# Kernel optimization log

Measured on AMD Instinct MI355X. Metric: run time of the kernel, lower is better.

The kernel has to match this reference:

```python
import jax, jax.numpy as jnp
import numpy as np

D = 256
H = 8
DK = D // H
FF = 4 * D
EPS = 1e-5


def layer_norm(x, g, b):
    mu = jnp.mean(x, axis=-1, keepdims=True)
    var = jnp.mean(jnp.square(x - mu), axis=-1, keepdims=True)
    return (x - mu) * jax.lax.rsqrt(var + EPS) * g + b


def setup_inputs() -> dict:
    key = jax.random.key(0)
    ks = jax.random.split(key, 12)
    s = 0.02
    return {
        "x": jax.random.normal(ks[0], (4, 2048, D), jnp.float32),
        "Wq": jax.random.normal(ks[1], (D, D), jnp.float32) * s,
        "Wk": jax.random.normal(ks[2], (D, D), jnp.float32) * s,
        "Wv": jax.random.normal(ks[3], (D, D), jnp.float32) * s,
        "Wo": jax.random.normal(ks[4], (D, D), jnp.float32) * s,
        "W1": jax.random.normal(ks[5], (D, FF), jnp.float32) * s,
        "W2": jax.random.normal(ks[6], (D, FF), jnp.float32) * s,
        "Wout": jax.random.normal(ks[7], (FF, D), jnp.float32) * s,
        "g1": jnp.ones((D,), jnp.float32),
        "b1": jnp.zeros((D,), jnp.float32),
        "g2": jnp.ones((D,), jnp.float32),
        "b2": jnp.zeros((D,), jnp.float32),
    }


def reference(x, Wq, Wk, Wv, Wo, W1, W2, Wout, g1, b1, g2, b2):
    B, S, _ = x.shape
    # --- multi-head attention (manual matmul + softmax + matmul) ---
    q = (x @ Wq).reshape(B, S, H, DK).transpose(0, 2, 1, 3)  # [B,H,S,DK]
    k = (x @ Wk).reshape(B, S, H, DK).transpose(0, 2, 1, 3)
    v = (x @ Wv).reshape(B, S, H, DK).transpose(0, 2, 1, 3)
    scores = jnp.einsum("bhqd,bhkd->bhqk", q, k) * (DK ** -0.5)  # [B,H,S,S]
    probs = jax.nn.softmax(scores, axis=-1)
    o = jnp.einsum("bhqk,bhkd->bhqd", probs, v)
    attn = o.transpose(0, 2, 1, 3).reshape(B, S, D) @ Wo
    # --- GLU feedforward with dual LayerNorms ---
    x1 = layer_norm(x + attn, g1, b1)
    xw = jax.nn.silu(x1 @ W1)
    xv = x1 @ W2
    out = (xw * xv) @ Wout
    return layer_norm(x1 + out, g2, b2)
```

## Files before the change

kernel.cpp:

```cpp
#include <hip/hip_runtime.h>

#define D 256
#define H 8
#define DK 32
#define FF 1024
#define SEQ 2048
#define BATCH 4
#define MROWS (BATCH * SEQ)
#define LN_EPS 1e-5f
#define QSCALE (0.1767766952966369f * 1.4426950408889634f)
#define LOG2E 1.4426950408889634f

typedef unsigned short u16;
typedef unsigned int u32;
typedef __attribute__((ext_vector_type(8))) short bf16x8;
typedef __attribute__((ext_vector_type(4))) float f32x4;

#define MFMA16(a, b, c) __builtin_amdgcn_mfma_f32_16x16x32_bf16(a, b, c, 0, 0, 0)

#if __has_builtin(__builtin_amdgcn_exp2f)
#define EXP2(x) __builtin_amdgcn_exp2f(x)
#else
#define EXP2(x) exp2f(x)
#endif
#if __has_builtin(__builtin_amdgcn_rcpf)
#define RCPF(x) __builtin_amdgcn_rcpf(x)
#else
#define RCPF(x) (1.f / (x))
#endif

__device__ __forceinline__ u16 f2bf(float f) {
    union { float f; u32 u; } x; x.f = f;
    u32 r = x.u + 0x7fffu + ((x.u >> 16) & 1u);
    return (u16)(r >> 16);
}
__device__ __forceinline__ u32 pack2(float a, float b) {
    return (u32)f2bf(a) | ((u32)f2bf(b) << 16);
}
__device__ __forceinline__ u32 pktrunc(float a, float b) {
    u32 ua = __builtin_bit_cast(u32, a), ub = __builtin_bit_cast(u32, b);
    return __builtin_amdgcn_perm(ub, ua, 0x07060302u);
}
__device__ __forceinline__ float silu_f(float x) {
    return x * RCPF(1.f + EXP2(-x * LOG2E));
}

__global__ void stage_w(const float* __restrict__ Wq, const float* __restrict__ Wk,
                        const float* __restrict__ Wv, const float* __restrict__ Wo,
                        const float* __restrict__ W1, const float* __restrict__ W2,
                        const float* __restrict__ Wout, u16* __restrict__ dst) {
    __shared__ float T[64][65];
    int bid = blockIdx.x, tid = threadIdx.x;
    const float* src;
    size_t dbase;
    int K, N, tile;
    float sc = 1.f;
    if (bid < 64) {
        int which = bid >> 4;
        tile = bid & 15;
        src = which == 0 ? Wq : which == 1 ? Wk : which == 2 ? Wv : Wo;
        if (which == 0) sc = QSCALE;
        dbase = (size_t)which << 16;
        K = 256; N = 256;
    } else if (bid < 192) {
        int which = (bid - 64) >> 6;
        tile = (bid - 64) & 63;
        src = which ? W2 : W1;
        dbase = 262144 + (size_t)which * 262144;
        K = 256; N = 1024;
    } else {
        tile = bid - 192;
        src = Wout;
        dbase = 786432;
        K = 1024; N = 256;
    }
    int ntn = N >> 6;
    int k0 = (tile / ntn) << 6, n0 = (tile % ntn) << 6;
#pragma unroll
    for (int p = 0; p < 4; p++) {
        int r = p * 16 + (tid >> 4), c = (tid & 15) * 4;
        float4 v = *(const float4*)(src + (size_t)(k0 + r) * N + n0 + c);
        T[c + 0][r] = v.x * sc;
        T[c + 1][r] = v.y * sc;
        T[c + 2][r] = v.z * sc;
        T[c + 3][r] = v.w * sc;
    }
    __syncthreads();
#pragma unroll
    for (int p = 0; p < 4; p++) {
        int n = p * 16 + (tid >> 4), k = (tid & 15) * 4;
        uint2 o;
        o.x = pack2(T[n][k], T[n][k + 1]);
        o.y = pack2(T[n][k + 2], T[n][k + 3]);
        *(uint2*)(dst + dbase + (size_t)(n0 + n) * K + k0 + k) = o;
    }
}

__global__ __launch_bounds__(512, 3)
void gemm_qkv(const float* __restrict__ X, const u16* __restrict__ Bt,
              u16* __restrict__ Qo, u16* __restrict__ Ko,
              u16* __restrict__ Vo) {
    __shared__ __align__(16) u16 WL[64][260];
    int tid = threadIdx.x;
    int w = tid >> 6, lane = tid & 63;
    int m = lane & 15, quad = lane >> 4;
    int cg = blockIdx.x % 12, rg = blockIdx.x / 12;
    int n0 = cg << 6;
#pragma unroll
    for (int i = 0; i < 4; i++) {
        int idx = i * 512 + tid;
        int row = idx >> 5, seg = idx & 31;
        *(uint4*)(&WL[row][seg * 8]) =
            *(const uint4*)(Bt + (size_t)(n0 + row) * D + seg * 8);
    }
    __syncthreads();
    int m0 = rg * 128 + w * 16;
    const float* xp = X + (size_t)(m0 + m) * D + quad * 8;
    f32x4 acc[4] = {{0,0,0,0},{0,0,0,0},{0,0,0,0},{0,0,0,0}};
#pragma unroll
    for (int k0 = 0; k0 < D; k0 += 32) {
        float4 f0 = *(const float4*)(xp + k0);
        float4 f1 = *(const float4*)(xp + k0 + 4);
        uint4 u0;
        u0.x = pktrunc(f0.x, f0.y); u0.y = pktrunc(f0.z, f0.w);
        u0.z = pktrunc(f1.x, f1.y); u0.w = pktrunc(f1.z, f1.w);
        bf16x8 a0 = __builtin_bit_cast(bf16x8, u0);
#pragma unroll
        for (int t = 0; t < 4; t++) {
            bf16x8 bv = *(const bf16x8*)(&WL[t * 16 + m][k0 + quad * 8]);
            acc[t] = MFMA16(a0, bv, acc[t]);
        }
    }
    int seg = cg >> 2;
    int nc0 = (cg & 3) << 6;
    int row = m0 + (quad << 2);
    if (seg < 2) {
        u16* out = seg ? Ko : Qo;
#pragma unroll
        for (int t = 0; t < 4; t++) {
            int col = nc0 + t * 16 + m;
#pragma unroll
            for (int r = 0; r < 4; r++)
                out[(size_t)(row + r) * D + col] = f2bf(acc[t][r]);
        }
    } else {
        int b = row >> 11, sl = row & 2047;
#pragma unroll
        for (int t = 0; t < 4; t++) {
            int col = nc0 + t * 16 + m;
            int hh = col >> 5, dk = col & 31;
            size_t base = ((size_t)(b * 8 + hh) * 32 + dk) * SEQ + sl;
            uint2 pk;
            pk.x = pack2(acc[t][0], acc[t][1]);
            pk.y = pack2(acc[t][2], acc[t][3]);
            *(uint2*)(Vo + base) = pk;
        }
    }
}

__global__ __launch_bounds__(256, 8)
void attn_mfma(const u16* __restrict__ Q, const u16* __restrict__ Km,
               const u16* __restrict__ Vt, u16* __restrict__ O) {
    __shared__ __align__(16) u16 Kt[2][64][36];
    __shared__ __align__(16) u16 Vl[2][32][68];
    int tid = threadIdx.x;
    int lane = tid & 63;
    int m = lane & 15, quad = lane >> 4;
    int w = tid >> 6;
    int bid = blockIdx.x;
    int qb = bid & 63;
    int bh = bid >> 6;
    int b = bh >> 3, h = bh & 7;
    int q0 = qb * 32 + (w & 1) * 16;
    int hb = w >> 1;
    size_t rowbase = (size_t)b * SEQ;

    bf16x8 qa = *(const bf16x8*)(Q + (rowbase + q0 + m) * D + h * DK + quad * 8);

    const u16* kg = Km + rowbase * D + h * DK;
    const u16* vg = Vt + (size_t)bh * DK * SEQ;

    int krow = tid >> 2, kseg = tid & 3;
    int skv = (krow & 32) | (((krow >> 2) & 3) << 3) | (((krow >> 4) & 1) << 2) | (krow & 3);
    int vrow = tid >> 3, vseg = tid & 7;

    uint4 kreg = *(const uint4*)(kg + (size_t)skv * D + kseg * 8);
    uint4 vreg = *(const uint4*)(vg + (size_t)vrow * SEQ + vseg * 8);
    *(uint4*)(&Kt[0][krow][kseg * 8]) = kreg;
    *(uint4*)(&Vl[0][vrow][vseg * 8]) = vreg;

    f32x4 o0 = {0,0,0,0}, o1 = {0,0,0,0};
    float ls = 0.f;

    for (int i = 0; i < SEQ / 64; i++) {
        int buf = i & 1;
        if (i + 1 < SEQ / 64) {
            int kvn = (i + 1) * 64;
            kreg = *(const uint4*)(kg + (size_t)(kvn + skv) * D + kseg * 8);
            vreg = *(const uint4*)(vg + (size_t)vrow * SEQ + kvn + vseg * 8);
        }
        __syncthreads();
        f32x4 z = {0,0,0,0};
        f32x4 s0, s1;
        {
            bf16x8 kb0 = *(const bf16x8*)(&Kt[buf][(2 * hb) * 16 + m][quad * 8]);
            bf16x8 kb1 = *(const bf16x8*)(&Kt[buf][(2 * hb + 1) * 16 + m][quad * 8]);
            s0 = MFMA16(kb0, qa, z);
            s1 = MFMA16(kb1, qa, z);
        }
        {
            float pa0 = EXP2(s0[0]), pa1 = EXP2(s0[1]);
            float pa2 = EXP2(s0[2]), pa3 = EXP2(s0[3]);
            float pb0 = EXP2(s1[0]), pb1 = EXP2(s1[1]);
            float pb2 = EXP2(s1[2]), pb3 = EXP2(s1[3]);
            ls += ((pa0 + pa1) + (pa2 + pa3)) + ((pb0 + pb1) + (pb2 + pb3));
            uint4 pw;
            pw.x = pktrunc(pa0, pa1);
            pw.y = pktrunc(pa2, pa3);
            pw.z = pktrunc(pb0, pb1);
            pw.w = pktrunc(pb2, pb3);
            bf16x8 pfrag = __builtin_bit_cast(bf16x8, pw);
            bf16x8 vb0 = *(const bf16x8*)(&Vl[buf][m][hb * 32 + quad * 8]);
            bf16x8 vb1 = *(const bf16x8*)(&Vl[buf][16 + m][hb * 32 + quad * 8]);
            o0 = MFMA16(pfrag, vb0, o0);
            o1 = MFMA16(pfrag, vb1, o1);
        }
        if (i + 1 < SEQ / 64) {
            *(uint4*)(&Kt[buf ^ 1][krow][kseg * 8]) = kreg;
            *(uint4*)(&Vl[buf ^ 1][vrow][vseg * 8]) = vreg;
        }
    }
    ls += __shfl_xor(ls, 16);
    ls += __shfl_xor(ls, 32);
    __syncthreads();
    float* comb = (float*)&Kt[0][0][0];
    if (w >= 2) {
        float* c = comb + ((size_t)(w - 2) * 64 + lane) * 9;
#pragma unroll
        for (int r = 0; r < 4; r++) { c[r] = o0[r]; c[4 + r] = o1[r]; }
        c[8] = ls;
    }
    __syncthreads();
    if (w < 2) {
        const float* c = comb + ((size_t)w * 64 + lane) * 9;
#pragma unroll
        for (int r = 0; r < 4; r++) { o0[r] += c[r]; o1[r] += c[4 + r]; }
        ls += c[8];
        u16* ob = O + (rowbase + q0 + quad * 4) * D + h * DK;
#pragma unroll
        for (int r = 0; r < 4; r++) {
            float lr = __shfl(ls, quad * 4 + r);
            float inv = 1.f / lr;
            ob[(size_t)r * D + m] = f2bf(o0[r] * inv);
            ob[(size_t)r * D + 16 + m] = f2bf(o1[r] * inv);
        }
    }
}

__global__ __launch_bounds__(256, 2)
void wo_res_ln(const u16* __restrict__ A, const u16* __restrict__ Bt,
               const float* __restrict__ res, const float* __restrict__ g,
               const float* __restrict__ bb, float* __restrict__ outf,
               u16* __restrict__ outb) {
    __shared__ float Sy[4][16], Sq[4][16], Mu[16], Rs[16];
    int tid = threadIdx.x;
    int w = tid >> 6, lane = tid & 63;
    int m = lane & 15, quad = lane >> 4;
    int m0 = blockIdx.x << 4, n0 = w << 6;
    const u16* ap = A + (size_t)(m0 + m) * D + quad * 8;
    const u16* bp = Bt + (size_t)(n0 + m) * D + quad * 8;
    f32x4 acc[4] = {{0,0,0,0},{0,0,0,0},{0,0,0,0},{0,0,0,0}};
#pragma unroll
    for (int k0 = 0; k0 < D; k0 += 32) {
        bf16x8 a0 = *(const bf16x8*)(ap + k0);
#pragma unroll
        for (int t = 0; t < 4; t++)
            acc[t] = MFMA16(a0, *(const bf16x8*)(bp + (size_t)t * 16 * D + k0), acc[t]);
    }
#pragma unroll
    for (int r = 0; r < 4; r++) {
        int row = (quad << 2) + r;
        float sy = 0.f, sq = 0.f;
#pragma unroll
        for (int t = 0; t < 4; t++) {
            float y = acc[t][r] + res[(size_t)(m0 + row) * D + n0 + t * 16 + m];
            acc[t][r] = y;
            sy += y;
            sq += y * y;
        }
        sy += __shfl_xor(sy, 1); sq += __shfl_xor(sq, 1);
        sy += __shfl_xor(sy, 2); sq += __shfl_xor(sq, 2);
        sy += __shfl_xor(sy, 4); sq += __shfl_xor(sq, 4);
        sy += __shfl_xor(sy, 8); sq += __shfl_xor(sq, 8);
        if (m == 0) { Sy[w][row] = sy; Sq[w][row] = sq; }
    }
    __syncthreads();
    if (tid < 16) {
        float s = Sy[0][tid] + Sy[1][tid] + Sy[2][tid] + Sy[3][tid];
        float q = Sq[0][tid] + Sq[1][tid] + Sq[2][tid] + Sq[3][tid];
        float mu = s * (1.f / 256.f);
        float var = q * (1.f / 256.f) - mu * mu;
        Mu[tid] = mu;
        Rs[tid] = rsqrtf(var + LN_EPS);
    }
    __syncthreads();
#pragma unroll
    for (int r = 0; r < 4; r++) {
        int row = (quad << 2) + r;
        float mu = Mu[row], rs = Rs[row];
#pragma unroll
        for (int t = 0; t < 4; t++) {
            int col = n0 + t * 16 + m;
            float yv = (acc[t][r] - mu) * rs * g[col] + bb[col];
            outf[(size_t)(m0 + row) * D + col] = yv;
            outb[(size_t)(m0 + row) * D + col] = f2bf(yv);
        }
    }
}

__global__ __launch_bounds__(512, 2)
void glu_ws(const u16* __restrict__ x1b, const u16* __restrict__ W1t,
            const u16* __restrict__ W2t, u16* __restrict__ G) {
    __shared__ __align__(16) u16 WL[2][64][260];
    int tid = threadIdx.x;
    int w = tid >> 6, lane = tid & 63;
    int m = lane & 15, quad = lane >> 4;
    int cg = blockIdx.x & 15, rg = blockIdx.x >> 4;
    int n0 = cg << 6;
#pragma unroll
    for (int i = 0; i < 4; i++) {
        int idx = i * 512 + tid;
        int row = idx >> 5, seg = idx & 31;
        *(uint4*)(&WL[0][row][seg * 8]) =
            *(const uint4*)(W1t + (size_t)(n0 + row) * D + seg * 8);
        *(uint4*)(&WL[1][row][seg * 8]) =
            *(const uint4*)(W2t + (size_t)(n0 + row) * D + seg * 8);
    }
    __syncthreads();
    int mr = rg * 512 + w * 64;
    f32x4 a1[4][4], a2[4][4];
#pragma unroll
    for (int u = 0; u < 4; u++)
#pragma unroll
        for (int t = 0; t < 4; t++) {
            a1[u][t] = (f32x4){0.f, 0.f, 0.f, 0.f};
            a2[u][t] = (f32x4){0.f, 0.f, 0.f, 0.f};
        }
#pragma unroll
    for (int k0 = 0; k0 < D; k0 += 32) {
        bf16x8 av[4];
#pragma unroll
        for (int u = 0; u < 4; u++)
            av[u] = *(const bf16x8*)(x1b + (size_t)(mr + u * 16 + m) * D + k0 + quad * 8);
#pragma unroll
        for (int t = 0; t < 4; t++) {
            bf16x8 w1 = *(const bf16x8*)(&WL[0][t * 16 + m][k0 + quad * 8]);
            bf16x8 w2 = *(const bf16x8*)(&WL[1][t * 16 + m][k0 + quad * 8]);
#pragma unroll
            for (int u = 0; u < 4; u++) {
                a1[u][t] = MFMA16(av[u], w1, a1[u][t]);
                a2[u][t] = MFMA16(av[u], w2, a2[u][t]);
            }
        }
    }
#pragma unroll
    for (int u = 0; u < 4; u++) {
        int row = mr + u * 16 + (quad << 2);
#pragma unroll
        for (int t = 0; t < 4; t++) {
            int col = n0 + t * 16 + m;
#pragma unroll
            for (int r = 0; r < 4; r++)
                G[(size_t)(row + r) * FF + col] = f2bf(silu_f(a1[u][t][r]) * a2[u][t][r]);
        }
    }
}

__global__ __launch_bounds__(1024, 4)
void wout_ln(const u16* __restrict__ G, const u16* __restrict__ Woutt,
             const float* __restrict__ x1f, const float* __restrict__ g,
             const float* __restrict__ bb, float* __restrict__ outf) {
    __shared__ __align__(16) u16 Gl[32][1044];
    __shared__ float Sy[16][32], Sq[16][32], Mu[32], Rs[32];
    int tid = threadIdx.x;
    int w = tid >> 6, lane = tid & 63;
    int m = lane & 15, quad = lane >> 4;
    int m0 = blockIdx.x << 5;
#pragma unroll
    for (int i = 0; i < 4; i++) {
        int idx = i * 1024 + tid;
        int row = idx >> 7, seg = idx & 127;
        *(uint4*)(&Gl[row][seg * 8]) =
            *(const uint4*)(G + (size_t)(m0 + row) * FF + seg * 8);
    }
    __syncthreads();
    int n0p = w << 4;
    const u16* bp = Woutt + (size_t)(n0p + m) * FF + quad * 8;
    f32x4 acc[2] = {{0,0,0,0},{0,0,0,0}};
#pragma unroll 4
    for (int k0 = 0; k0 < FF; k0 += 32) {
        bf16x8 a0 = *(const bf16x8*)(&Gl[m][k0 + quad * 8]);
        bf16x8 a1v = *(const bf16x8*)(&Gl[16 + m][k0 + quad * 8]);
        bf16x8 bv = *(const bf16x8*)(bp + k0);
        acc[0] = MFMA16(a0, bv, acc[0]);
        acc[1] = MFMA16(a1v, bv, acc[1]);
    }
#pragma unroll
    for (int u = 0; u < 2; u++) {
#pragma unroll
        for (int r = 0; r < 4; r++) {
            int row = u * 16 + (quad << 2) + r;
            float y = acc[u][r] + x1f[(size_t)(m0 + row) * D + n0p + m];
            acc[u][r] = y;
            float sy = y, sq = y * y;
            sy += __shfl_xor(sy, 1); sq += __shfl_xor(sq, 1);
            sy += __shfl_xor(sy, 2); sq += __shfl_xor(sq, 2);
            sy += __shfl_xor(sy, 4); sq += __shfl_xor(sq, 4);
            sy += __shfl_xor(sy, 8); sq += __shfl_xor(sq, 8);
            if (m == 0) { Sy[w][row] = sy; Sq[w][row] = sq; }
        }
    }
    __syncthreads();
    if (tid < 32) {
        float s = 0.f, q = 0.f;
#pragma unroll
        for (int ww = 0; ww < 16; ww++) { s += Sy[ww][tid]; q += Sq[ww][tid]; }
        float mu = s * (1.f / 256.f);
        float var = q * (1.f / 256.f) - mu * mu;
        Mu[tid] = mu;
        Rs[tid] = rsqrtf(var + LN_EPS);
    }
    __syncthreads();
#pragma unroll
    for (int u = 0; u < 2; u++) {
#pragma unroll
        for (int r = 0; r < 4; r++) {
            int row = u * 16 + (quad << 2) + r;
            int col = n0p + m;
            outf[(size_t)(m0 + row) * D + col] =
                (acc[u][r] - Mu[row]) * Rs[row] * g[col] + bb[col];
        }
    }
}

#define WS_WQKVT  ((size_t)0)
#define WS_WOT    ((size_t)196608)
#define WS_W1T    ((size_t)262144)
#define WS_W2T    ((size_t)524288)
#define WS_WOUTT  ((size_t)786432)
#define WS_Q      ((size_t)1048576)
#define WS_K      ((size_t)3145728)
#define WS_VT     ((size_t)5242880)
#define WS_O      ((size_t)7340032)
#define WS_GATED  ((size_t)1048576)
#define WS_X1F    ((size_t)9437184)
#define WS_X1B    ((size_t)13631488)

extern "C" void kernel_launch(void* const* d_in, const int* in_sizes, int n_in,
                              void* d_out, int out_size, void* d_ws, size_t ws_size,
                              hipStream_t stream) {
    const float* x    = (const float*)d_in[0];
    const float* Wq   = (const float*)d_in[1];
    const float* Wk   = (const float*)d_in[2];
    const float* Wv   = (const float*)d_in[3];
    const float* Wo   = (const float*)d_in[4];
    const float* W1   = (const float*)d_in[5];
    const float* W2   = (const float*)d_in[6];
    const float* Wout = (const float*)d_in[7];
    const float* g1   = (const float*)d_in[8];
    const float* b1   = (const float*)d_in[9];
    const float* g2   = (const float*)d_in[10];
    const float* b2   = (const float*)d_in[11];

    u16* ws = (u16*)d_ws;
    float* x1f = (float*)(ws + WS_X1F);

    stage_w<<<256, 256, 0, stream>>>(Wq, Wk, Wv, Wo, W1, W2, Wout, ws + WS_WQKVT);

    gemm_qkv<<<768, 512, 0, stream>>>(x, ws + WS_WQKVT,
                                      ws + WS_Q, ws + WS_K, ws + WS_VT);

    attn_mfma<<<2048, 256, 0, stream>>>(ws + WS_Q, ws + WS_K, ws + WS_VT, ws + WS_O);

    wo_res_ln<<<512, 256, 0, stream>>>(ws + WS_O, ws + WS_WOT, x, g1, b1,
                                       x1f, ws + WS_X1B);

    glu_ws<<<256, 512, 0, stream>>>(ws + WS_X1B, ws + WS_W1T, ws + WS_W2T,
                                    ws + WS_GATED);

    wout_ln<<<256, 1024, 0, stream>>>(ws + WS_GATED, ws + WS_WOUTT, x1f,
                                      g2, b2, (float*)d_out);
}
```

Measured before the change: 184.0 us.

## Process 64 query rows per attention block to reuse K/V tiles

Each attention warp now handles two 16-row query fragments instead of one, so every block covers 64 queries and the grid is halved. Each K/V tile staged in shared memory feeds twice as many MFMAs, which halves global K/V traffic and the number of per-tile syncs. The trade-off is more registers per thread, which may lower occupancy under the existing launch bounds, plus a larger cross-wave combine buffer in shared memory.

```diff
diff --git a/kernel.cpp b/kernel.cpp
--- a/kernel.cpp
+++ b/kernel.cpp
@@ -168,14 +168,15 @@
     int m = lane & 15, quad = lane >> 4;
     int w = tid >> 6;
     int bid = blockIdx.x;
-    int qb = bid & 63;
-    int bh = bid >> 6;
+    int qb = bid & 31;
+    int bh = bid >> 5;
     int b = bh >> 3, h = bh & 7;
-    int q0 = qb * 32 + (w & 1) * 16;
+    int q0 = qb * 64 + (w & 1) * 32;
     int hb = w >> 1;
     size_t rowbase = (size_t)b * SEQ;
 
-    bf16x8 qa = *(const bf16x8*)(Q + (rowbase + q0 + m) * D + h * DK + quad * 8);
+    bf16x8 qa0 = *(const bf16x8*)(Q + (rowbase + q0 + m) * D + h * DK + quad * 8);
+    bf16x8 qa1 = *(const bf16x8*)(Q + (rowbase + q0 + 16 + m) * D + h * DK + quad * 8);
 
     const u16* kg = Km + rowbase * D + h * DK;
     const u16* vg = Vt + (size_t)bh * DK * SEQ;
@@ -190,7 +191,8 @@
     *(uint4*)(&Vl[0][vrow][vseg * 8]) = vreg;
 
     f32x4 o0 = {0,0,0,0}, o1 = {0,0,0,0};
-    float ls = 0.f;
+    f32x4 o2 = {0,0,0,0}, o3 = {0,0,0,0};
+    float ls0 = 0.f, ls1 = 0.f;
 
     for (int i = 0; i < SEQ / 64; i++) {
         int buf = i & 1;
@@ -201,58 +203,82 @@
         }
         __syncthreads();
         f32x4 z = {0,0,0,0};
-        f32x4 s0, s1;
-        {
-            bf16x8 kb0 = *(const bf16x8*)(&Kt[buf][(2 * hb) * 16 + m][quad * 8]);
-            bf16x8 kb1 = *(const bf16x8*)(&Kt[buf][(2 * hb + 1) * 16 + m][quad * 8]);
-            s0 = MFMA16(kb0, qa, z);
-            s1 = MFMA16(kb1, qa, z);
-        }
+        bf16x8 kb0 = *(const bf16x8*)(&Kt[buf][(2 * hb) * 16 + m][quad * 8]);
+        bf16x8 kb1 = *(const bf16x8*)(&Kt[buf][(2 * hb + 1) * 16 + m][quad * 8]);
+        f32x4 s0 = MFMA16(kb0, qa0, z);
+        f32x4 s1 = MFMA16(kb1, qa0, z);
+        f32x4 s2 = MFMA16(kb0, qa1, z);
+        f32x4 s3 = MFMA16(kb1, qa1, z);
+        bf16x8 vb0 = *(const bf16x8*)(&Vl[buf][m][hb * 32 + quad * 8]);
+        bf16x8 vb1 = *(const bf16x8*)(&Vl[buf][16 + m][hb * 32 + quad * 8]);
         {
             float pa0 = EXP2(s0[0]), pa1 = EXP2(s0[1]);
             float pa2 = EXP2(s0[2]), pa3 = EXP2(s0[3]);
             float pb0 = EXP2(s1[0]), pb1 = EXP2(s1[1]);
             float pb2 = EXP2(s1[2]), pb3 = EXP2(s1[3]);
-            ls += ((pa0 + pa1) + (pa2 + pa3)) + ((pb0 + pb1) + (pb2 + pb3));
+            ls0 += ((pa0 + pa1) + (pa2 + pa3)) + ((pb0 + pb1) + (pb2 + pb3));
             uint4 pw;
             pw.x = pktrunc(pa0, pa1);
             pw.y = pktrunc(pa2, pa3);
             pw.z = pktrunc(pb0, pb1);
             pw.w = pktrunc(pb2, pb3);
-            bf16x8 pfrag = __builtin_bit_cast(bf16x8, pw);
-            bf16x8 vb0 = *(const bf16x8*)(&Vl[buf][m][hb * 32 + quad * 8]);
-            bf16x8 vb1 = *(const bf16x8*)(&Vl[buf][16 + m][hb * 32 + quad * 8]);
-            o0 = MFMA16(pfrag, vb0, o0);
-            o1 = MFMA16(pfrag, vb1, o1);
+            bf16x8 pf = __builtin_bit_cast(bf16x8, pw);
+            o0 = MFMA16(pf, vb0, o0);
+            o1 = MFMA16(pf, vb1, o1);
+        }
+        {
+            float pa0 = EXP2(s2[0]), pa1 = EXP2(s2[1]);
+            float pa2 = EXP2(s2[2]), pa3 = EXP2(s2[3]);
+            float pb0 = EXP2(s3[0]), pb1 = EXP2(s3[1]);
+            float pb2 = EXP2(s3[2]), pb3 = EXP2(s3[3]);
+            ls1 += ((pa0 + pa1) + (pa2 + pa3)) + ((pb0 + pb1) + (pb2 + pb3));
+            uint4 pw;
+            pw.x = pktrunc(pa0, pa1);
+            pw.y = pktrunc(pa2, pa3);
+            pw.z = pktrunc(pb0, pb1);
+            pw.w = pktrunc(pb2, pb3);
+            bf16x8 pf = __builtin_bit_cast(bf16x8, pw);
+            o2 = MFMA16(pf, vb0, o2);
+            o3 = MFMA16(pf, vb1, o3);
         }
         if (i + 1 < SEQ / 64) {
             *(uint4*)(&Kt[buf ^ 1][krow][kseg * 8]) = kreg;
             *(uint4*)(&Vl[buf ^ 1][vrow][vseg * 8]) = vreg;
         }
     }
-    ls += __shfl_xor(ls, 16);
-    ls += __shfl_xor(ls, 32);
+    ls0 += __shfl_xor(ls0, 16); ls0 += __shfl_xor(ls0, 32);
+    ls1 += __shfl_xor(ls1, 16); ls1 += __shfl_xor(ls1, 32);
     __syncthreads();
     float* comb = (float*)&Kt[0][0][0];
     if (w >= 2) {
-        float* c = comb + ((size_t)(w - 2) * 64 + lane) * 9;
-#pragma unroll
-        for (int r = 0; r < 4; r++) { c[r] = o0[r]; c[4 + r] = o1[r]; }
-        c[8] = ls;
+        float* c = comb + ((size_t)(w - 2) * 64 + lane) * 18;
+#pragma unroll
+        for (int r = 0; r < 4; r++) {
+            c[r] = o0[r]; c[4 + r] = o1[r];
+            c[8 + r] = o2[r]; c[12 + r] = o3[r];
+        }
+        c[16] = ls0; c[17] = ls1;
     }
     __syncthreads();
     if (w < 2) {
-        const float* c = comb + ((size_t)w * 64 + lane) * 9;
-#pragma unroll
-        for (int r = 0; r < 4; r++) { o0[r] += c[r]; o1[r] += c[4 + r]; }
-        ls += c[8];
-        u16* ob = O + (rowbase + q0 + quad * 4) * D + h * DK;
+        const float* c = comb + ((size_t)w * 64 + lane) * 18;
 #pragma unroll
         for (int r = 0; r < 4; r++) {
-            float lr = __shfl(ls, quad * 4 + r);
-            float inv = 1.f / lr;
-            ob[(size_t)r * D + m] = f2bf(o0[r] * inv);
-            ob[(size_t)r * D + 16 + m] = f2bf(o1[r] * inv);
+            o0[r] += c[r]; o1[r] += c[4 + r];
+            o2[r] += c[8 + r]; o3[r] += c[12 + r];
+        }
+        ls0 += c[16]; ls1 += c[17];
+        u16* ob0 = O + (rowbase + q0 + quad * 4) * D + h * DK;
+        u16* ob1 = O + (rowbase + q0 + 16 + quad * 4) * D + h * DK;
+#pragma unroll
+        for (int r = 0; r < 4; r++) {
+            float l0 = __shfl(ls0, quad * 4 + r);
+            float l1 = __shfl(ls1, quad * 4 + r);
+            float i0 = 1.f / l0, i1 = 1.f / l1;
+            ob0[(size_t)r * D + m] = f2bf(o0[r] * i0);
+            ob0[(size_t)r * D + 16 + m] = f2bf(o1[r] * i0);
+            ob1[(size_t)r * D + m] = f2bf(o2[r] * i1);
+            ob1[(size_t)r * D + 16 + m] = f2bf(o3[r] * i1);
         }
     }
 }
@@ -480,7 +506,7 @@
     gemm_qkv<<<768, 512, 0, stream>>>(x, ws + WS_WQKVT,
                                       ws + WS_Q, ws + WS_K, ws + WS_VT);
 
-    attn_mfma<<<2048, 256, 0, stream>>>(ws + WS_Q, ws + WS_K, ws + WS_VT, ws + WS_O);
+    attn_mfma<<<1024, 256, 0, stream>>>(ws + WS_Q, ws + WS_K, ws + WS_VT, ws + WS_O);
 
     wo_res_ln<<<512, 256, 0, stream>>>(ws + WS_O, ws + WS_WOT, x, g1, b1,
                                        x1f, ws + WS_X1B);
```

After: 199.2 us. 8.2% more time.
